# Kernel optimization log

Measured on AMD Instinct MI355X. Metric: run time of the kernel, lower is better.

The kernel has to match this reference:

```python
import jax, jax.numpy as jnp
import numpy as np

E = 8          # num_tasks / experts (world_size=1 -> local_experts=E)
N = 8192       # tokens
H = 768        # hidden_size
I = 3072       # intermediate_size
EPS = 1e-12    # layer_norm_eps


def setup_inputs() -> dict:
    key = jax.random.key(0)
    ks = jax.random.split(key, 8)
    x = jax.random.normal(ks[0], (N, H), dtype=jnp.float32)
    # arange task ids -> hash (mod E) gives perfectly balanced expert loads
    task_ids = jnp.arange(N, dtype=jnp.int64)
    s1 = 1.0 / np.sqrt(H)
    s2 = 1.0 / np.sqrt(I)
    W1 = jax.random.uniform(ks[1], (E, H, I), jnp.float32, -s1, s1)
    b1 = jax.random.uniform(ks[2], (E, I), jnp.float32, -s1, s1)
    W2 = jax.random.uniform(ks[3], (E, I, H), jnp.float32, -s2, s2)
    b2 = jax.random.uniform(ks[4], (E, H), jnp.float32, -s2, s2)
    gamma = jnp.ones((E, H), jnp.float32)
    beta = jnp.zeros((E, H), jnp.float32)
    return {"x": x, "task_ids": task_ids, "W1": W1, "b1": b1,
            "W2": W2, "b2": b2, "gamma": gamma, "beta": beta}


def reference(x, task_ids, W1, b1, W2, b2, gamma, beta):
    # hash protocol: expert = task_id % num_experts
    expert = (task_ids % E).astype(jnp.int32)
    order = jnp.argsort(expert)              # dispatch (scatter router)
    C = N // E                               # balanced capacity per expert
    xs = x[order].reshape(E, C, H)           # [E, C, H] per-expert token blocks
    # per-expert FFN as grouped GEMMs
    h = jnp.einsum('ech,ehi->eci', xs, W1) + b1[:, None, :]
    h = jax.nn.gelu(h, approximate=False)
    y = jnp.einsum('eci,eih->ech', h, W2) + b2[:, None, :]
    # dropout is identity in eval; residual + per-expert LayerNorm
    z = y + xs
    mu = jnp.mean(z, axis=-1, keepdims=True)
    var = jnp.mean((z - mu) ** 2, axis=-1, keepdims=True)
    z = (z - mu) * jax.lax.rsqrt(var + EPS)
    z = z * gamma[:, None, :] + beta[:, None, :]
    # combine (gather router): undo the dispatch permutation
    out = jnp.zeros((N, H), x.dtype).at[order].set(z.reshape(N, H))
    return out
```

## Files before the change

kernel.cpp:

```cpp
#include <hip/hip_runtime.h>
#include <hip/hip_bf16.h>

#define NE   8
#define NTOK 8192
#define DH   768
#define DI   3072
#define CAP  1024

typedef __bf16 bf16x8 __attribute__((ext_vector_type(8)));
typedef float  f32x4  __attribute__((ext_vector_type(4)));

__device__ __forceinline__ void gload_lds16(const void* g, void* l) {
  __builtin_amdgcn_global_load_lds(
      (const __attribute__((address_space(1))) unsigned int*)g,
      (__attribute__((address_space(3))) unsigned int*)l, 16, 0, 0);
}

__global__ __launch_bounds__(256)
void transpose_cvt(const float* __restrict__ in, __hip_bfloat16* __restrict__ out,
                   int R, int C) {
  __shared__ float lds[64 * 64];
  const int e = blockIdx.z;
  const float* src = in + (size_t)e * R * C;
  __hip_bfloat16* dst = out + (size_t)e * R * C;
  const int c0 = blockIdx.x * 64, r0 = blockIdx.y * 64;
  const int t = threadIdx.x;

  {
    const int rr = t >> 4;
    const int cq = t & 15;
#pragma unroll
    for (int j = 0; j < 4; ++j) {
      const int r = rr + 16 * j;
      const float4 v = *(const float4*)(src + (size_t)(r0 + r) * C + c0 + cq * 4);
      *(float4*)&lds[r * 64 + ((cq ^ ((r >> 3) & 7)) << 2)] = v;
    }
  }
  __syncthreads();
  {
    const int r8 = (t & 7) * 8;
    const int cb = t >> 3;
#pragma unroll
    for (int j = 0; j < 2; ++j) {
      const int c = cb + 32 * j;
      __hip_bfloat16 tmp[8];
#pragma unroll
      for (int i = 0; i < 8; ++i) {
        const int rr = r8 + i;
        tmp[i] = __float2bfloat16(
            lds[rr * 64 + ((((c >> 2) ^ ((rr >> 3) & 7)) << 2) | (c & 3))]);
      }
      *(uint4*)(dst + (size_t)(c0 + c) * R + r0 + r8) = *(const uint4*)tmp;
    }
  }
}

__global__ __launch_bounds__(256)
void gather_cvt_x(const float* __restrict__ x, __hip_bfloat16* __restrict__ xs) {
  const int j = blockIdx.x * 256 + threadIdx.x;
  const int orow = j / 96;
  const int k8 = (j - orow * 96) * 8;
  const int e = orow >> 10, c = orow & 1023;
  const int tok = c * 8 + e;
  const float4* p = (const float4*)(x + (size_t)tok * DH + k8);
  float4 u = p[0], v = p[1];
  __hip_bfloat16 tmp[8];
  tmp[0] = __float2bfloat16(u.x); tmp[1] = __float2bfloat16(u.y);
  tmp[2] = __float2bfloat16(u.z); tmp[3] = __float2bfloat16(u.w);
  tmp[4] = __float2bfloat16(v.x); tmp[5] = __float2bfloat16(v.y);
  tmp[6] = __float2bfloat16(v.z); tmp[7] = __float2bfloat16(v.w);
  *(uint4*)(xs + (size_t)orow * DH + k8) = *(const uint4*)tmp;
}

template <int EPI>
__global__ __launch_bounds__(256)
void gemm_bt(const __hip_bfloat16* __restrict__ A,
             const __hip_bfloat16* __restrict__ Bt,
             const float* __restrict__ bias,
             void* __restrict__ OutP,
             int N, int K, int KK, int gx, int gy, int nsplit,
             size_t sAe, size_t sBe, size_t sOe, int sBias, size_t sSplit) {
  __shared__ __hip_bfloat16 As[128 * 64];
  __shared__ __hip_bfloat16 Bs[128 * 64];

  const int nblk = gridDim.x;
  const int chunk = nblk >> 3;
  const int id = (blockIdx.x & 7) * chunk + (blockIdx.x >> 3);
  const int per_e = gx * gy * nsplit;
  const int e = id / per_e;
  int r = id - e * per_e;
  const int s = r / (gx * gy);
  r -= s * (gx * gy);
  const int bx = r / gy;
  const int by = r - bx * gy;

  const int t = threadIdx.x;
  const int lane = t & 63;
  const int w = t >> 6;
  const int g = lane >> 4;
  const int l15 = lane & 15;
  const int wm = w >> 1, wn = w & 1;

  const __hip_bfloat16* Ae = A + (size_t)e * sAe + (size_t)by * 128 * K;
  const __hip_bfloat16* Be = Bt + (size_t)e * sBe + (size_t)bx * 128 * K;

  const int rowStg = t >> 3;
  const int srcOff = ((t & 7) ^ (rowStg & 7)) * 8;
  const size_t stgBase = (size_t)rowStg * K + srcOff;

  f32x4 acc[4][4] = {};

  for (int kt = 0; kt < KK; ++kt) {
    const int k0 = (s * KK + kt) * 64;
#pragma unroll
    for (int i = 0; i < 4; ++i) {
      gload_lds16(Ae + stgBase + (size_t)i * 32 * K + k0, (char*)As + (i * 256 + t) * 16);
      gload_lds16(Be + stgBase + (size_t)i * 32 * K + k0, (char*)Bs + (i * 256 + t) * 16);
    }
    __syncthreads();
#pragma unroll
    for (int ks = 0; ks < 2; ++ks) {
      bf16x8 af[4], bv[4];
#pragma unroll
      for (int fm = 0; fm < 4; ++fm) {
        const int rA = wm * 64 + fm * 16 + l15;
        af[fm] = *(const bf16x8*)((const char*)As + rA * 128 + ((ks * 4 + g) ^ (rA & 7)) * 16);
      }
#pragma unroll
      for (int fn = 0; fn < 4; ++fn) {
        const int rB = wn * 64 + fn * 16 + l15;
        bv[fn] = *(const bf16x8*)((const char*)Bs + rB * 128 + ((ks * 4 + g) ^ (rB & 7)) * 16);
      }
#pragma unroll
      for (int fm = 0; fm < 4; ++fm)
#pragma unroll
        for (int fn = 0; fn < 4; ++fn)
          acc[fm][fn] = __builtin_amdgcn_mfma_f32_16x16x32_bf16(af[fm], bv[fn], acc[fm][fn], 0, 0, 0);
    }
    __syncthreads();
  }

  const float* biasE = bias + (size_t)e * sBias + bx * 128;
  if (EPI == 0) {
    __hip_bfloat16* O = (__hip_bfloat16*)OutP + (size_t)e * sOe +
                        (size_t)by * 128 * N + bx * 128;
#pragma unroll
    for (int fm = 0; fm < 4; ++fm)
#pragma unroll
      for (int fn = 0; fn < 4; ++fn) {
        const int n = wn * 64 + fn * 16 + l15;
        const float bvv = biasE[n];
#pragma unroll
        for (int rg = 0; rg < 4; ++rg) {
          const int m = wm * 64 + fm * 16 + g * 4 + rg;
          float v = acc[fm][fn][rg] + bvv;
          v = 0.5f * v * (1.0f + erff(v * 0.70710678118654752f));
          O[(size_t)m * N + n] = __float2bfloat16(v);
        }
      }
  } else {
    float* O = (float*)OutP + (size_t)s * sSplit + (size_t)e * sOe +
               (size_t)by * 128 * N + bx * 128;
#pragma unroll
    for (int fm = 0; fm < 4; ++fm)
#pragma unroll
      for (int fn = 0; fn < 4; ++fn) {
        const int n = wn * 64 + fn * 16 + l15;
        const float bvv = (s == 0) ? biasE[n] : 0.0f;
#pragma unroll
        for (int rg = 0; rg < 4; ++rg) {
          const int m = wm * 64 + fm * 16 + g * 4 + rg;
          O[(size_t)m * N + n] = acc[fm][fn][rg] + bvv;
        }
      }
  }
}

__global__ __launch_bounds__(256)
void resid_ln(const float* __restrict__ y0, const float* __restrict__ y1, int two,
              const float* __restrict__ x,
              const float* __restrict__ gamma, const float* __restrict__ beta,
              float* __restrict__ out) {
  const int row = blockIdx.x;
  const int e = row >> 10, c = row & 1023;
  const int tok = c * 8 + e;
  const float* y0r = y0 + (size_t)row * DH;
  const float* y1r = y1 + (size_t)row * DH;
  const float* xr = x + (size_t)tok * DH;
  const int t = threadIdx.x;
  float z[3];
  float s = 0.f, s2 = 0.f;
#pragma unroll
  for (int j = 0; j < 3; ++j) {
    float v = y0r[t + 256 * j] + xr[t + 256 * j];
    if (two) v += y1r[t + 256 * j];
    z[j] = v; s += v; s2 += v * v;
  }
#pragma unroll
  for (int off = 32; off; off >>= 1) {
    s += __shfl_down(s, off);
    s2 += __shfl_down(s2, off);
  }
  __shared__ float rs[4], rs2[4];
  if ((t & 63) == 0) { rs[t >> 6] = s; rs2[t >> 6] = s2; }
  __syncthreads();
  const float S = rs[0] + rs[1] + rs[2] + rs[3];
  const float S2 = rs2[0] + rs2[1] + rs2[2] + rs2[3];
  const float mu = S * (1.0f / DH);
  const float var = S2 * (1.0f / DH) - mu * mu;
  const float rstd = rsqrtf(var + 1e-12f);
  const float* ga = gamma + (size_t)e * DH;
  const float* be = beta + (size_t)e * DH;
  float* orow = out + (size_t)tok * DH;
#pragma unroll
  for (int j = 0; j < 3; ++j) {
    const int h = t + 256 * j;
    orow[h] = (z[j] - mu) * rstd * ga[h] + be[h];
  }
}

extern "C" void kernel_launch(void* const* d_in, const int* in_sizes, int n_in,
                              void* d_out, int out_size, void* d_ws, size_t ws_size,
                              hipStream_t stream) {
  const float* x     = (const float*)d_in[0];
  const float* W1    = (const float*)d_in[2];
  const float* b1    = (const float*)d_in[3];
  const float* W2    = (const float*)d_in[4];
  const float* b2    = (const float*)d_in[5];
  const float* gamma = (const float*)d_in[6];
  const float* beta  = (const float*)d_in[7];
  float* out = (float*)d_out;

  char* base = (char*)d_ws;
  __hip_bfloat16* W1t  = (__hip_bfloat16*)base;
  __hip_bfloat16* W2t  = (__hip_bfloat16*)(base + 37748736ull);
  __hip_bfloat16* hbuf = (__hip_bfloat16*)(base + 75497472ull);
  __hip_bfloat16* xs   = (__hip_bfloat16*)(base + 125829120ull);
  float* y0 = (float*)xs;
  float* y1 = (float*)(base + 150994944ull);
  const int nsplit = (ws_size >= 176160768ull) ? 2 : 1;

  transpose_cvt<<<dim3(DI / 64, DH / 64, NE), 256, 0, stream>>>(W1, W1t, DH, DI);
  transpose_cvt<<<dim3(DH / 64, DI / 64, NE), 256, 0, stream>>>(W2, W2t, DI, DH);
  gather_cvt_x<<<(NTOK * (DH / 8)) / 256, 256, 0, stream>>>(x, xs);

  gemm_bt<0><<<(DI / 128) * (CAP / 128) * NE, 256, 0, stream>>>(
      xs, W1t, b1, hbuf, DI, DH, DH / 64, DI / 128, CAP / 128, 1,
      (size_t)CAP * DH, (size_t)DI * DH, (size_t)CAP * DI, DI, 0);

  gemm_bt<1><<<(DH / 128) * (CAP / 128) * NE * nsplit, 256, 0, stream>>>(
      hbuf, W2t, b2, y0, DH, DI, DI / 64 / nsplit, DH / 128, CAP / 128, nsplit,
      (size_t)CAP * DI, (size_t)DH * DI, (size_t)CAP * DH, DH, (size_t)NTOK * DH);

  resid_ln<<<NTOK, 256, 0, stream>>>(y0, y1, nsplit - 1, x, gamma, beta, out);
}
```

Baseline: 349.7 us.

## Pipeline GEMMs with triple-buffered LDS, 512 threads, fused prep kernel, tanh GELU

Replaces the single-buffered GEMM with a triple-buffered direct-to-LDS pipeline that prefetches two k-tiles ahead, uses 512 threads per block with an 8-wave layout, and raises MFMA priority with setprio. The three weight/input conversion kernels are merged into one launch. The split-K output for the second GEMM always goes to a second buffer aliased onto the W1t workspace. Exact erf GELU is replaced by a tanh-approximation via sigmoid, which changes numerics slightly.

```diff
diff --git a/kernel.cpp b/kernel.cpp
--- a/kernel.cpp
+++ b/kernel.cpp
@@ -16,30 +16,31 @@
       (__attribute__((address_space(3))) unsigned int*)l, 16, 0, 0);
 }
 
-__global__ __launch_bounds__(256)
-void transpose_cvt(const float* __restrict__ in, __hip_bfloat16* __restrict__ out,
-                   int R, int C) {
+__device__ __forceinline__ void transpose_body(const float* __restrict__ src,
+                                               __hip_bfloat16* __restrict__ dst,
+                                               int R, int C, int bb) {
   __shared__ float lds[64 * 64];
-  const int e = blockIdx.z;
-  const float* src = in + (size_t)e * R * C;
-  __hip_bfloat16* dst = out + (size_t)e * R * C;
-  const int c0 = blockIdx.x * 64, r0 = blockIdx.y * 64;
+  const int gx = C >> 6, gyc = R >> 6;
+  const int cx = bb % gx;
+  const int rem = bb / gx;
+  const int ry = rem % gyc;
+  const int e = rem / gyc;
+  const float* s = src + (size_t)e * R * C;
+  __hip_bfloat16* d = dst + (size_t)e * R * C;
+  const int c0 = cx * 64, r0 = ry * 64;
   const int t = threadIdx.x;
-
   {
-    const int rr = t >> 4;
-    const int cq = t & 15;
+    const int rr = t >> 4, cq = t & 15;
 #pragma unroll
     for (int j = 0; j < 4; ++j) {
       const int r = rr + 16 * j;
-      const float4 v = *(const float4*)(src + (size_t)(r0 + r) * C + c0 + cq * 4);
+      const float4 v = *(const float4*)(s + (size_t)(r0 + r) * C + c0 + cq * 4);
       *(float4*)&lds[r * 64 + ((cq ^ ((r >> 3) & 7)) << 2)] = v;
     }
   }
   __syncthreads();
   {
-    const int r8 = (t & 7) * 8;
-    const int cb = t >> 3;
+    const int r8 = (t & 7) * 8, cb = t >> 3;
 #pragma unroll
     for (int j = 0; j < 2; ++j) {
       const int c = cb + 32 * j;
@@ -50,14 +51,20 @@
         tmp[i] = __float2bfloat16(
             lds[rr * 64 + ((((c >> 2) ^ ((rr >> 3) & 7)) << 2) | (c & 3))]);
       }
-      *(uint4*)(dst + (size_t)(c0 + c) * R + r0 + r8) = *(const uint4*)tmp;
+      *(uint4*)(d + (size_t)(c0 + c) * R + r0 + r8) = *(const uint4*)tmp;
     }
   }
 }
 
 __global__ __launch_bounds__(256)
-void gather_cvt_x(const float* __restrict__ x, __hip_bfloat16* __restrict__ xs) {
-  const int j = blockIdx.x * 256 + threadIdx.x;
+void prep(const float* __restrict__ W1, const float* __restrict__ W2,
+          const float* __restrict__ x,
+          __hip_bfloat16* __restrict__ W1t, __hip_bfloat16* __restrict__ W2t,
+          __hip_bfloat16* __restrict__ xs) {
+  const int b = blockIdx.x;
+  if (b < 4608) { transpose_body(W1, W1t, DH, DI, b); return; }
+  if (b < 9216) { transpose_body(W2, W2t, DI, DH, b - 4608); return; }
+  const int j = (b - 9216) * 256 + threadIdx.x;
   const int orow = j / 96;
   const int k8 = (j - orow * 96) * 8;
   const int e = orow >> 10, c = orow & 1023;
@@ -73,15 +80,14 @@
 }
 
 template <int EPI>
-__global__ __launch_bounds__(256)
-void gemm_bt(const __hip_bfloat16* __restrict__ A,
-             const __hip_bfloat16* __restrict__ Bt,
-             const float* __restrict__ bias,
-             void* __restrict__ OutP,
-             int N, int K, int KK, int gx, int gy, int nsplit,
-             size_t sAe, size_t sBe, size_t sOe, int sBias, size_t sSplit) {
-  __shared__ __hip_bfloat16 As[128 * 64];
-  __shared__ __hip_bfloat16 Bs[128 * 64];
+__global__ __launch_bounds__(512, 1)
+void gemm_pipe(const __hip_bfloat16* __restrict__ A,
+               const __hip_bfloat16* __restrict__ Bt,
+               const float* __restrict__ bias,
+               void* __restrict__ OutP,
+               int N, int K, int KK, int gx, int gy, int nsplit,
+               size_t sAe, size_t sBe, size_t sOe, int sBias, long long sSplit) {
+  __shared__ char sh[3 * 32768];
 
   const int nblk = gridDim.x;
   const int chunk = nblk >> 3;
@@ -89,8 +95,7 @@
   const int per_e = gx * gy * nsplit;
   const int e = id / per_e;
   int r = id - e * per_e;
-  const int s = r / (gx * gy);
-  r -= s * (gx * gy);
+  const int s = r / (gx * gy); r -= s * (gx * gy);
   const int bx = r / gy;
   const int by = r - bx * gy;
 
@@ -99,46 +104,75 @@
   const int w = t >> 6;
   const int g = lane >> 4;
   const int l15 = lane & 15;
-  const int wm = w >> 1, wn = w & 1;
+  const int wm = w >> 2, wn = w & 3;
 
   const __hip_bfloat16* Ae = A + (size_t)e * sAe + (size_t)by * 128 * K;
   const __hip_bfloat16* Be = Bt + (size_t)e * sBe + (size_t)bx * 128 * K;
 
   const int rowStg = t >> 3;
-  const int srcOff = ((t & 7) ^ (rowStg & 7)) * 8;
-  const size_t stgBase = (size_t)rowStg * K + srcOff;
-
-  f32x4 acc[4][4] = {};
-
-  for (int kt = 0; kt < KK; ++kt) {
-    const int k0 = (s * KK + kt) * 64;
-#pragma unroll
-    for (int i = 0; i < 4; ++i) {
-      gload_lds16(Ae + stgBase + (size_t)i * 32 * K + k0, (char*)As + (i * 256 + t) * 16);
-      gload_lds16(Be + stgBase + (size_t)i * 32 * K + k0, (char*)Bs + (i * 256 + t) * 16);
+  const size_t stgA = (size_t)rowStg * K + ((t & 7) ^ (rowStg & 7)) * 8 + s * KK * 64;
+
+#define STAGE(kt, b) do {                                                       \
+    const int k0_ = (kt) * 64;                                                  \
+    _Pragma("unroll")                                                           \
+    for (int i_ = 0; i_ < 2; ++i_) {                                            \
+      gload_lds16(Ae + stgA + (size_t)i_ * 64 * K + k0_,                        \
+                  sh + (b) * 32768 + (i_ * 512 + t) * 16);                      \
+      gload_lds16(Be + stgA + (size_t)i_ * 64 * K + k0_,                        \
+                  sh + (b) * 32768 + 16384 + (i_ * 512 + t) * 16);              \
+    }                                                                           \
+  } while (0)
+
+  f32x4 acc[4][2] = {};
+  const int rA0 = wm * 64 + l15;
+  const int rB0 = wn * 32 + l15;
+
+#define COMPUTE(b) do {                                                         \
+    const char* Ab_ = sh + (b) * 32768;                                         \
+    const char* Bb_ = Ab_ + 16384;                                              \
+    _Pragma("unroll")                                                           \
+    for (int ks = 0; ks < 2; ++ks) {                                            \
+      bf16x8 af[4], bv[2];                                                      \
+      _Pragma("unroll")                                                         \
+      for (int fm = 0; fm < 4; ++fm) {                                          \
+        const int rr = rA0 + fm * 16;                                           \
+        af[fm] = *(const bf16x8*)(Ab_ + rr * 128 + ((ks * 4 + g) ^ (rr & 7)) * 16); \
+      }                                                                         \
+      _Pragma("unroll")                                                         \
+      for (int fn = 0; fn < 2; ++fn) {                                          \
+        const int rr = rB0 + fn * 16;                                           \
+        bv[fn] = *(const bf16x8*)(Bb_ + rr * 128 + ((ks * 4 + g) ^ (rr & 7)) * 16); \
+      }                                                                         \
+      __builtin_amdgcn_s_setprio(1);                                            \
+      _Pragma("unroll")                                                         \
+      for (int fm = 0; fm < 4; ++fm)                                            \
+        _Pragma("unroll")                                                       \
+        for (int fn = 0; fn < 2; ++fn)                                          \
+          acc[fm][fn] = __builtin_amdgcn_mfma_f32_16x16x32_bf16(af[fm], bv[fn], acc[fm][fn], 0, 0, 0); \
+      __builtin_amdgcn_s_setprio(0);                                            \
+    }                                                                           \
+  } while (0)
+
+  STAGE(0, 0);
+  STAGE(1, 1);
+  int bc = 0;
+  for (int kt = 0; kt < KK - 1; ++kt) {
+    asm volatile("s_waitcnt vmcnt(4)" ::: "memory");
+    __builtin_amdgcn_sched_barrier(0);
+    __builtin_amdgcn_s_barrier();
+    if (kt + 2 < KK) {
+      const int bs = bc >= 1 ? bc - 1 : 2;
+      STAGE(kt + 2, bs);
     }
-    __syncthreads();
-#pragma unroll
-    for (int ks = 0; ks < 2; ++ks) {
-      bf16x8 af[4], bv[4];
-#pragma unroll
-      for (int fm = 0; fm < 4; ++fm) {
-        const int rA = wm * 64 + fm * 16 + l15;
-        af[fm] = *(const bf16x8*)((const char*)As + rA * 128 + ((ks * 4 + g) ^ (rA & 7)) * 16);
-      }
-#pragma unroll
-      for (int fn = 0; fn < 4; ++fn) {
-        const int rB = wn * 64 + fn * 16 + l15;
-        bv[fn] = *(const bf16x8*)((const char*)Bs + rB * 128 + ((ks * 4 + g) ^ (rB & 7)) * 16);
-      }
-#pragma unroll
-      for (int fm = 0; fm < 4; ++fm)
-#pragma unroll
-        for (int fn = 0; fn < 4; ++fn)
-          acc[fm][fn] = __builtin_amdgcn_mfma_f32_16x16x32_bf16(af[fm], bv[fn], acc[fm][fn], 0, 0, 0);
-    }
-    __syncthreads();
-  }
+    COMPUTE(bc);
+    bc = bc == 2 ? 0 : bc + 1;
+  }
+  asm volatile("s_waitcnt vmcnt(0)" ::: "memory");
+  __builtin_amdgcn_sched_barrier(0);
+  __builtin_amdgcn_s_barrier();
+  COMPUTE(bc);
+#undef STAGE
+#undef COMPUTE
 
   const float* biasE = bias + (size_t)e * sBias + bx * 128;
   if (EPI == 0) {
@@ -147,25 +181,26 @@
 #pragma unroll
     for (int fm = 0; fm < 4; ++fm)
 #pragma unroll
-      for (int fn = 0; fn < 4; ++fn) {
-        const int n = wn * 64 + fn * 16 + l15;
+      for (int fn = 0; fn < 2; ++fn) {
+        const int n = wn * 32 + fn * 16 + l15;
         const float bvv = biasE[n];
 #pragma unroll
         for (int rg = 0; rg < 4; ++rg) {
           const int m = wm * 64 + fm * 16 + g * 4 + rg;
           float v = acc[fm][fn][rg] + bvv;
-          v = 0.5f * v * (1.0f + erff(v * 0.70710678118654752f));
+          const float z = 1.5957691216057308f * (v + 0.044715f * v * v * v);
+          v = v / (1.0f + __expf(-z));
           O[(size_t)m * N + n] = __float2bfloat16(v);
         }
       }
   } else {
-    float* O = (float*)OutP + (size_t)s * sSplit + (size_t)e * sOe +
+    float* O = (float*)OutP + (long long)s * sSplit + (size_t)e * sOe +
                (size_t)by * 128 * N + bx * 128;
 #pragma unroll
     for (int fm = 0; fm < 4; ++fm)
 #pragma unroll
-      for (int fn = 0; fn < 4; ++fn) {
-        const int n = wn * 64 + fn * 16 + l15;
+      for (int fn = 0; fn < 2; ++fn) {
+        const int n = wn * 32 + fn * 16 + l15;
         const float bvv = (s == 0) ? biasE[n] : 0.0f;
 #pragma unroll
         for (int rg = 0; rg < 4; ++rg) {
@@ -177,7 +212,7 @@
 }
 
 __global__ __launch_bounds__(256)
-void resid_ln(const float* __restrict__ y0, const float* __restrict__ y1, int two,
+void resid_ln(const float* __restrict__ y0, const float* __restrict__ y1,
               const float* __restrict__ x,
               const float* __restrict__ gamma, const float* __restrict__ beta,
               float* __restrict__ out) {
@@ -192,8 +227,7 @@
   float s = 0.f, s2 = 0.f;
 #pragma unroll
   for (int j = 0; j < 3; ++j) {
-    float v = y0r[t + 256 * j] + xr[t + 256 * j];
-    if (two) v += y1r[t + 256 * j];
+    const float v = y0r[t + 256 * j] + y1r[t + 256 * j] + xr[t + 256 * j];
     z[j] = v; s += v; s2 += v * v;
   }
 #pragma unroll
@@ -237,20 +271,18 @@
   __hip_bfloat16* hbuf = (__hip_bfloat16*)(base + 75497472ull);
   __hip_bfloat16* xs   = (__hip_bfloat16*)(base + 125829120ull);
   float* y0 = (float*)xs;
-  float* y1 = (float*)(base + 150994944ull);
-  const int nsplit = (ws_size >= 176160768ull) ? 2 : 1;
-
-  transpose_cvt<<<dim3(DI / 64, DH / 64, NE), 256, 0, stream>>>(W1, W1t, DH, DI);
-  transpose_cvt<<<dim3(DH / 64, DI / 64, NE), 256, 0, stream>>>(W2, W2t, DI, DH);
-  gather_cvt_x<<<(NTOK * (DH / 8)) / 256, 256, 0, stream>>>(x, xs);
-
-  gemm_bt<0><<<(DI / 128) * (CAP / 128) * NE, 256, 0, stream>>>(
-      xs, W1t, b1, hbuf, DI, DH, DH / 64, DI / 128, CAP / 128, 1,
+  float* y1 = (float*)base;
+
+  prep<<<12288, 256, 0, stream>>>(W1, W2, x, W1t, W2t, xs);
+
+  gemm_pipe<0><<<24 * 8 * NE, 512, 0, stream>>>(
+      xs, W1t, b1, hbuf, DI, DH, DH / 64, 24, 8, 1,
       (size_t)CAP * DH, (size_t)DI * DH, (size_t)CAP * DI, DI, 0);
 
-  gemm_bt<1><<<(DH / 128) * (CAP / 128) * NE * nsplit, 256, 0, stream>>>(
-      hbuf, W2t, b2, y0, DH, DI, DI / 64 / nsplit, DH / 128, CAP / 128, nsplit,
-      (size_t)CAP * DI, (size_t)DH * DI, (size_t)CAP * DH, DH, (size_t)NTOK * DH);
-
-  resid_ln<<<NTOK, 256, 0, stream>>>(y0, y1, nsplit - 1, x, gamma, beta, out);
-}
+  gemm_pipe<1><<<6 * 8 * NE * 2, 512, 0, stream>>>(
+      hbuf, W2t, b2, y0, DH, DI, DI / 64 / 2, 6, 8, 2,
+      (size_t)CAP * DI, (size_t)DH * DI, (size_t)CAP * DH, DH,
+      (long long)(y1 - y0));
+
+  resid_ln<<<NTOK, 256, 0, stream>>>(y0, y1, x, gamma, beta, out);
+}
```

Result: slower. 358.7 us (+2.6%).
